# Kernel optimization log

Measured on AMD Instinct MI355X. Metric: run time of the kernel, lower is better.

Reference implementation:

```python
import jax, jax.numpy as jnp
import numpy as np

B, S, D = 1, 2048, 1024
E, F, TOP_K = 8, 2048, 2
LN_EPS = 1e-5


def setup_inputs() -> dict:
    key = jax.random.key(0)
    ks = jax.random.split(key, 8)
    sc_in = 1.0 / np.sqrt(D)
    sc_hid = 1.0 / np.sqrt(F)
    return {
        "x": jax.random.normal(ks[0], (B, S, D), dtype=jnp.float32),
        "Wr": jax.random.normal(ks[1], (D, E), dtype=jnp.float32) * sc_in,
        "br": jnp.zeros((E,), dtype=jnp.float32),
        "W1": jax.random.normal(ks[2], (E, D, F), dtype=jnp.float32) * sc_in,
        "b1": jnp.zeros((E, F), dtype=jnp.float32),
        "W2": jax.random.normal(ks[3], (E, F, D), dtype=jnp.float32) * sc_hid,
        "b2": jnp.zeros((E, D), dtype=jnp.float32),
        "gamma": jnp.ones((D,), dtype=jnp.float32),
        "beta": jnp.zeros((D,), dtype=jnp.float32),
    }


def reference(x, Wr, br, W1, b1, W2, b2, gamma, beta):
    # x: (B, S, D)
    xf = x.reshape(-1, D)  # (T, D), T = B*S
    # Router: softmax over expert logits, then top-k scores/indices.
    probs = jax.nn.softmax(xf @ Wr + br, axis=-1)           # (T, E)
    scores, idx = jax.lax.top_k(probs, TOP_K)               # (T, K)
    # combine[t, e] = sum_k scores[t, k] * [idx[t, k] == e]  (weighted scatter)
    onehot = jax.nn.one_hot(idx, E, dtype=xf.dtype)         # (T, K, E)
    combine = jnp.einsum('tk,tke->te', scores, onehot)      # (T, E)
    # Per-expert FFN, weighted scatter-add combine. Tokens not routed to an
    # expert have combine weight 0 -> identical math to masked gather/scatter.
    out = jnp.zeros_like(xf)
    for e in range(E):  # E is a small static constant
        h = jax.nn.gelu(xf @ W1[e] + b1[e])                 # (T, F)
        out = out + combine[:, e:e + 1] * (h @ W2[e] + b2[e])
    # Residual + LayerNorm (dropout = 0)
    y = x + out.reshape(B, S, D)
    mu = jnp.mean(y, axis=-1, keepdims=True)
    var = jnp.mean(jnp.square(y - mu), axis=-1, keepdims=True)
    return (y - mu) * jax.lax.rsqrt(var + LN_EPS) * gamma + beta
```

## Files before the change

### kernel.cpp

```cpp
#include <hip/hip_runtime.h>

#define T_TOK 2048
#define DDIM  1024
#define EEXP  8
#define FDIM  2048

typedef __attribute__((ext_vector_type(8))) short bf16x8;
typedef __attribute__((ext_vector_type(4))) float f32x4;
typedef __attribute__((ext_vector_type(4))) unsigned short u16x4;

__device__ __forceinline__ unsigned short f2bf(float f) {
  union { float f; unsigned int u; } v; v.f = f;
  unsigned int r = v.u + 0x7FFF + ((v.u >> 16) & 1);
  return (unsigned short)(r >> 16);
}
__device__ __forceinline__ float gelu_tanh(float x) {
  const float c = 0.7978845608028654f;
  float t = c * (x + 0.044715f * x * x * x);
  return 0.5f * x * (1.0f + tanhf(t));
}
__device__ __forceinline__ void gload_lds16(const void* g, void* lds) {
  __builtin_amdgcn_global_load_lds(
      (const __attribute__((address_space(1))) void*)g,
      (__attribute__((address_space(3))) void*)lds, 16, 0, 0);
}

__global__ __launch_bounds__(256)
void router_kernel(const float* __restrict__ x, const float* __restrict__ Wr,
                   const float* __restrict__ br, float* __restrict__ combine,
                   unsigned short* __restrict__ xbf) {
  int t = blockIdx.x;
  int tid = threadIdx.x;
  float acc[EEXP];
#pragma unroll
  for (int e = 0; e < EEXP; ++e) acc[e] = 0.f;
  const float* xr = x + (size_t)t * DDIM;
  unsigned short* xbr = xbf + (size_t)t * DDIM;
  for (int d = tid; d < DDIM; d += 256) {
    float xv = xr[d];
    xbr[d] = f2bf(xv);
    const float* w = Wr + d * EEXP;
#pragma unroll
    for (int e = 0; e < EEXP; ++e) acc[e] += xv * w[e];
  }
#pragma unroll
  for (int e = 0; e < EEXP; ++e)
    for (int off = 32; off > 0; off >>= 1) acc[e] += __shfl_down(acc[e], off);
  __shared__ float red[4][EEXP];
  int wave = tid >> 6, lane = tid & 63;
  if (lane == 0)
#pragma unroll
    for (int e = 0; e < EEXP; ++e) red[wave][e] = acc[e];
  __syncthreads();
  if (tid == 0) {
    float l[EEXP];
#pragma unroll
    for (int e = 0; e < EEXP; ++e)
      l[e] = red[0][e] + red[1][e] + red[2][e] + red[3][e] + br[e];
    int i0 = 0;
    for (int e = 1; e < EEXP; ++e) if (l[e] > l[i0]) i0 = e;
    int i1 = -1;
    for (int e = 0; e < EEXP; ++e) {
      if (e == i0) continue;
      if (i1 < 0 || l[e] > l[i1]) i1 = e;
    }
    float m = l[0];
    for (int e = 1; e < EEXP; ++e) m = fmaxf(m, l[e]);
    float p[EEXP], s = 0.f;
#pragma unroll
    for (int e = 0; e < EEXP; ++e) { p[e] = __expf(l[e] - m); s += p[e]; }
    float inv = 1.0f / s;
#pragma unroll
    for (int e = 0; e < EEXP; ++e)
      combine[t * EEXP + e] = (e == i0 || e == i1) ? p[e] * inv : 0.0f;
  }
}

__global__ __launch_bounds__(512)
void compact_kernel(const float* __restrict__ combine, int* __restrict__ idx,
                    int* __restrict__ meta) {
  int e = threadIdx.x >> 6, lane = threadIdx.x & 63;
  int cnt = 0;
  for (int t0 = 0; t0 < T_TOK; t0 += 64) {
    int t = t0 + lane;
    bool f = combine[t * EEXP + e] != 0.0f;
    unsigned long long m = __ballot(f);
    if (f) idx[e * T_TOK + cnt + __popcll(m & ((1ull << lane) - 1))] = t;
    cnt += __popcll(m);
  }
  __shared__ int sc[EEXP];
  if (lane == 0) sc[e] = cnt;
  __syncthreads();
  if (threadIdx.x == 0) {
    int b = 0;
    for (int i = 0; i < EEXP; ++i) { meta[i] = sc[i]; meta[8 + i] = b; b += sc[i]; }
    meta[16] = b;
  }
}

__global__ __launch_bounds__(256)
void wconv_kernel(const float* __restrict__ W1, const float* __restrict__ W2,
                  unsigned short* __restrict__ W1t, unsigned short* __restrict__ W2t) {
  __shared__ float tile[32][33];
  int z = blockIdx.z;
  const float* in; unsigned short* out; int R, C;
  if (z < 8) { in = W1 + (size_t)z * DDIM * FDIM; out = W1t + (size_t)z * DDIM * FDIM; R = DDIM; C = FDIM; }
  else       { in = W2 + (size_t)(z - 8) * DDIM * FDIM; out = W2t + (size_t)(z - 8) * DDIM * FDIM; R = FDIM; C = DDIM; }
  int tilesC = C >> 5;
  int tr = blockIdx.x / tilesC, tc = blockIdx.x % tilesC;
  int r0 = tr << 5, c0 = tc << 5;
  int t = threadIdx.x;
  int lr = t >> 3, lc4 = (t & 7) << 2;
  const float4 v = *(const float4*)(in + (size_t)(r0 + lr) * C + c0 + lc4);
  tile[lr][lc4 + 0] = v.x; tile[lr][lc4 + 1] = v.y;
  tile[lr][lc4 + 2] = v.z; tile[lr][lc4 + 3] = v.w;
  __syncthreads();
  u16x4 o;
  o[0] = f2bf(tile[lc4 + 0][lr]);
  o[1] = f2bf(tile[lc4 + 1][lr]);
  o[2] = f2bf(tile[lc4 + 2][lr]);
  o[3] = f2bf(tile[lc4 + 3][lr]);
  *(u16x4*)(out + (size_t)(c0 + lr) * R + r0 + lc4) = o;
}

template<int EPI>
__global__ __launch_bounds__(256)
void gemm_kernel(const unsigned short* __restrict__ A,
                 const unsigned short* __restrict__ Ball,
                 const float* __restrict__ ball,
                 const float* __restrict__ combine,
                 const int* __restrict__ idx,
                 const int* __restrict__ meta,
                 unsigned short* __restrict__ Hc,
                 float* __restrict__ accum) {
  constexpr int KF = (EPI == 0) ? DDIM : FDIM;
  constexpr int N  = (EPI == 0) ? FDIM : DDIM;
  constexpr int NT = 16;
  __shared__ unsigned short Asub[2 * 128 * 64];
  __shared__ unsigned short Bsub[2 * 128 * 64];

  int id = blockIdx.x;
  int a = id >> 7, rem = id & 127;
  int mtile = rem >> 3, b = rem & 7;
  int ne = a * 8 + b;
  int nsl = ne & 15, e = ne >> 4;
  int ntile, kbeg;
  if (EPI == 0) { ntile = nsl; kbeg = 0; }
  else          { ntile = nsl & 7; kbeg = (nsl >> 3) * 1024; }

  int cnt = meta[e];
  int m0 = mtile << 7;
  if (m0 >= cnt) return;
  int base = meta[8 + e];
  const unsigned short* B = Ball + (size_t)e * KF * N;
  const float* bias = ball + (size_t)e * N;
  int n0 = ntile << 7;
  int tid = threadIdx.x, wave = tid >> 6, lane = tid & 63;
  int wm = wave >> 1, wn = wave & 1;
  int lr = lane & 15, lk = lane >> 4;

  int arow[4], brow[4], scol[4];
#pragma unroll
  for (int i = 0; i < 4; ++i) {
    int phys = i * 4096 + wave * 1024 + lane * 16;
    int row = phys >> 7;
    int lc = (phys & 127) ^ ((row & 7) << 4);
    scol[i] = lc >> 1;
    int lrow = min(m0 + row, cnt - 1);
    arow[i] = (EPI == 0) ? idx[e * T_TOK + lrow] : (base + lrow);
    brow[i] = n0 + row;
  }

  auto stage = [&](int buf, int kt) {
#pragma unroll
    for (int i = 0; i < 4; ++i) {
      gload_lds16(A + (size_t)arow[i] * KF + kt + scol[i],
                  (char*)Asub + buf * 16384 + i * 4096 + wave * 1024);
      gload_lds16(B + (size_t)brow[i] * KF + kt + scol[i],
                  (char*)Bsub + buf * 16384 + i * 4096 + wave * 1024);
    }
  };

  f32x4 acc[4][4] = {};
  stage(0, kbeg);
  __syncthreads();
  int cur = 0;
  for (int t = 0; t < NT; ++t) {
    if (t + 1 < NT) stage(cur ^ 1, kbeg + (t + 1) * 64);
#pragma unroll
    for (int ks = 0; ks < 2; ++ks) {
      bf16x8 af[4], bf_[4];
#pragma unroll
      for (int m = 0; m < 4; ++m) {
        int row = wm * 64 + m * 16 + lr;
        int cb = (ks * 64 + lk * 16) ^ ((row & 7) << 4);
        af[m] = *(const bf16x8*)((const char*)Asub + cur * 16384 + row * 128 + cb);
      }
#pragma unroll
      for (int n = 0; n < 4; ++n) {
        int row = wn * 64 + n * 16 + lr;
        int cb = (ks * 64 + lk * 16) ^ ((row & 7) << 4);
        bf_[n] = *(const bf16x8*)((const char*)Bsub + cur * 16384 + row * 128 + cb);
      }
#pragma unroll
      for (int m = 0; m < 4; ++m)
#pragma unroll
        for (int n = 0; n < 4; ++n)
          acc[m][n] = __builtin_amdgcn_mfma_f32_16x16x32_bf16(af[m], bf_[n], acc[m][n], 0, 0, 0);
    }
    __syncthreads();
    cur ^= 1;
  }

  if (EPI == 0) {
#pragma unroll
    for (int m = 0; m < 4; ++m) {
      int lbase = m0 + wm * 64 + m * 16 + lk * 4;
#pragma unroll
      for (int n = 0; n < 4; ++n) {
        int col = n0 + wn * 64 + n * 16 + lr;
        float bv = bias[col];
#pragma unroll
        for (int r = 0; r < 4; ++r) {
          int local = lbase + r;
          if (local < cnt)
            Hc[(size_t)(base + local) * N + col] = f2bf(gelu_tanh(acc[m][n][r] + bv));
        }
      }
    }
  } else {
    bool addb = (kbeg == 0);
#pragma unroll
    for (int m = 0; m < 4; ++m) {
      int lbase = m0 + wm * 64 + m * 16 + lk * 4;
#pragma unroll
      for (int r = 0; r < 4; ++r) {
        int local = lbase + r;
        if (local < cnt) {
          int tok = idx[e * T_TOK + local];
          float c = combine[tok * EEXP + e];
#pragma unroll
          for (int n = 0; n < 4; ++n) {
            int col = n0 + wn * 64 + n * 16 + lr;
            float v = acc[m][n][r] + (addb ? bias[col] : 0.0f);
            atomicAdd(&accum[(size_t)tok * N + col], c * v);
          }
        }
      }
    }
  }
}

__global__ __launch_bounds__(256)
void ln_kernel(const float* __restrict__ x, const float* __restrict__ accum,
               const float* __restrict__ gamma, const float* __restrict__ beta,
               float* __restrict__ out) {
  int r = blockIdx.x, tid = threadIdx.x;
  size_t base = (size_t)r * DDIM + tid * 4;
  float4 xv = *(const float4*)(x + base);
  float4 av = *(const float4*)(accum + base);
  float y[4] = { xv.x + av.x, xv.y + av.y, xv.z + av.z, xv.w + av.w };
  float s = y[0] + y[1] + y[2] + y[3];
  float s2 = y[0] * y[0] + y[1] * y[1] + y[2] * y[2] + y[3] * y[3];
  for (int off = 32; off > 0; off >>= 1) {
    s += __shfl_down(s, off);
    s2 += __shfl_down(s2, off);
  }
  __shared__ float rs[4], rs2[4];
  int wave = tid >> 6, lane = tid & 63;
  if (lane == 0) { rs[wave] = s; rs2[wave] = s2; }
  __syncthreads();
  float ts = rs[0] + rs[1] + rs[2] + rs[3];
  float ts2 = rs2[0] + rs2[1] + rs2[2] + rs2[3];
  float mu = ts * (1.0f / DDIM);
  float var = ts2 * (1.0f / DDIM) - mu * mu;
  float inv = rsqrtf(var + 1e-5f);
  float4 gv = *(const float4*)(gamma + tid * 4);
  float4 bv = *(const float4*)(beta + tid * 4);
  float4 o;
  o.x = (y[0] - mu) * inv * gv.x + bv.x;
  o.y = (y[1] - mu) * inv * gv.y + bv.y;
  o.z = (y[2] - mu) * inv * gv.z + bv.z;
  o.w = (y[3] - mu) * inv * gv.w + bv.w;
  *(float4*)(out + base) = o;
}

#define BM 128
#define BN 128
#define BK 32
#define LDT 40

__global__ __launch_bounds__(256)
void g1_old(const float* __restrict__ X, const float* __restrict__ W1,
            const float* __restrict__ b1, unsigned short* __restrict__ H) {
  __shared__ unsigned short As[BM][LDT];
  __shared__ unsigned short Bs[BN][LDT];
  int tid = threadIdx.x;
  int trow0 = blockIdx.y * BM, ncol0 = blockIdx.x * BN;
  int wave = tid >> 6, lane = tid & 63;
  int wm = wave >> 1, wn = wave & 1;
  int lr = lane & 15, lk = lane >> 4;
  f32x4 acc[4][4] = {};
  for (int kt = 0; kt < DDIM; kt += BK) {
#pragma unroll
    for (int it = 0; it < 4; ++it) {
      int i = tid + it * 256;
      int row = i >> 3, c4 = (i & 7) << 2;
      const float4 v = *(const float4*)(X + (size_t)(trow0 + row) * DDIM + kt + c4);
      uint2 p;
      p.x = (unsigned int)f2bf(v.x) | ((unsigned int)f2bf(v.y) << 16);
      p.y = (unsigned int)f2bf(v.z) | ((unsigned int)f2bf(v.w) << 16);
      *(uint2*)&As[row][c4] = p;
    }
#pragma unroll
    for (int it = 0; it < 4; ++it) {
      int i = tid + it * 256;
      int r = i >> 5, c4 = (i & 31) << 2;
      const float4 v = *(const float4*)(W1 + (size_t)(kt + r) * FDIM + ncol0 + c4);
      Bs[c4 + 0][r] = f2bf(v.x); Bs[c4 + 1][r] = f2bf(v.y);
      Bs[c4 + 2][r] = f2bf(v.z); Bs[c4 + 3][r] = f2bf(v.w);
    }
    __syncthreads();
    bf16x8 af[4], bfr[4];
#pragma unroll
    for (int m = 0; m < 4; ++m) af[m] = *(const bf16x8*)&As[wm * 64 + m * 16 + lr][lk * 8];
#pragma unroll
    for (int n = 0; n < 4; ++n) bfr[n] = *(const bf16x8*)&Bs[wn * 64 + n * 16 + lr][lk * 8];
#pragma unroll
    for (int m = 0; m < 4; ++m)
#pragma unroll
      for (int n = 0; n < 4; ++n)
        acc[m][n] = __builtin_amdgcn_mfma_f32_16x16x32_bf16(af[m], bfr[n], acc[m][n], 0, 0, 0);
    __syncthreads();
  }
#pragma unroll
  for (int m = 0; m < 4; ++m) {
    int row = trow0 + wm * 64 + m * 16 + lk * 4;
#pragma unroll
    for (int n = 0; n < 4; ++n) {
      int col = ncol0 + wn * 64 + n * 16 + lr;
      float bv = b1[col];
#pragma unroll
      for (int r = 0; r < 4; ++r)
        H[(size_t)(row + r) * FDIM + col] = f2bf(gelu_tanh(acc[m][n][r] + bv));
    }
  }
}

__global__ __launch_bounds__(256)
void g2_old(const unsigned short* __restrict__ H, const float* __restrict__ W2,
            const float* __restrict__ b2, const float* __restrict__ combine,
            int e, float* __restrict__ out) {
  __shared__ unsigned short As[BM][LDT];
  __shared__ unsigned short Bs[BN][LDT];
  int tid = threadIdx.x;
  int trow0 = blockIdx.y * BM, ncol0 = blockIdx.x * BN;
  int wave = tid >> 6, lane = tid & 63;
  int wm = wave >> 1, wn = wave & 1;
  int lr = lane & 15, lk = lane >> 4;
  f32x4 acc[4][4] = {};
  for (int kt = 0; kt < FDIM; kt += BK) {
#pragma unroll
    for (int it = 0; it < 2; ++it) {
      int i = tid + it * 256;
      int row = i >> 2, c8 = (i & 3) << 3;
      uint4 v = *(const uint4*)(H + (size_t)(trow0 + row) * FDIM + kt + c8);
      *(uint4*)&As[row][c8] = v;
    }
#pragma unroll
    for (int it = 0; it < 4; ++it) {
      int i = tid + it * 256;
      int r = i >> 5, c4 = (i & 31) << 2;
      const float4 v = *(const float4*)(W2 + (size_t)(kt + r) * DDIM + ncol0 + c4);
      Bs[c4 + 0][r] = f2bf(v.x); Bs[c4 + 1][r] = f2bf(v.y);
      Bs[c4 + 2][r] = f2bf(v.z); Bs[c4 + 3][r] = f2bf(v.w);
    }
    __syncthreads();
    bf16x8 af[4], bfr[4];
#pragma unroll
    for (int m = 0; m < 4; ++m) af[m] = *(const bf16x8*)&As[wm * 64 + m * 16 + lr][lk * 8];
#pragma unroll
    for (int n = 0; n < 4; ++n) bfr[n] = *(const bf16x8*)&Bs[wn * 64 + n * 16 + lr][lk * 8];
#pragma unroll
    for (int m = 0; m < 4; ++m)
#pragma unroll
      for (int n = 0; n < 4; ++n)
        acc[m][n] = __builtin_amdgcn_mfma_f32_16x16x32_bf16(af[m], bfr[n], acc[m][n], 0, 0, 0);
    __syncthreads();
  }
#pragma unroll
  for (int m = 0; m < 4; ++m) {
    int row = trow0 + wm * 64 + m * 16 + lk * 4;
#pragma unroll
    for (int n = 0; n < 4; ++n) {
      int col = ncol0 + wn * 64 + n * 16 + lr;
      float bv = b2[col];
#pragma unroll
      for (int r = 0; r < 4; ++r) {
        int rr = row + r;
        float c = combine[rr * EEXP + e];
        if (c != 0.0f) out[(size_t)rr * DDIM + col] += c * (acc[m][n][r] + bv);
      }
    }
  }
}

extern "C" void kernel_launch(void* const* d_in, const int* in_sizes, int n_in,
                              void* d_out, int out_size, void* d_ws, size_t ws_size,
                              hipStream_t stream) {
  const float* x     = (const float*)d_in[0];
  const float* Wr    = (const float*)d_in[1];
  const float* br    = (const float*)d_in[2];
  const float* W1    = (const float*)d_in[3];
  const float* b1    = (const float*)d_in[4];
  const float* W2    = (const float*)d_in[5];
  const float* b2    = (const float*)d_in[6];
  const float* gamma = (const float*)d_in[7];
  const float* beta  = (const float*)d_in[8];

  size_t off_combine = 0;
  size_t off_meta    = off_combine + (size_t)T_TOK * EEXP * 4;
  size_t off_idx     = off_meta + 1024;
  size_t off_xbf     = off_idx + (size_t)EEXP * T_TOK * 4;
  size_t off_accum   = off_xbf + (size_t)T_TOK * DDIM * 2;
  size_t off_Hc      = off_accum + (size_t)T_TOK * DDIM * 4;
  size_t off_W1t     = off_Hc + (size_t)2 * T_TOK * FDIM * 2;
  size_t off_W2t     = off_W1t + (size_t)EEXP * DDIM * FDIM * 2;
  size_t need        = off_W2t + (size_t)EEXP * DDIM * FDIM * 2;

  float* combine = (float*)((char*)d_ws + off_combine);

  if (ws_size >= need) {
    int*   meta  = (int*)((char*)d_ws + off_meta);
    int*   idx   = (int*)((char*)d_ws + off_idx);
    unsigned short* xbf = (unsigned short*)((char*)d_ws + off_xbf);
    float* accum = (float*)((char*)d_ws + off_accum);
    unsigned short* Hc  = (unsigned short*)((char*)d_ws + off_Hc);
    unsigned short* W1t = (unsigned short*)((char*)d_ws + off_W1t);
    unsigned short* W2t = (unsigned short*)((char*)d_ws + off_W2t);

    wconv_kernel<<<dim3(2048, 1, 16), 256, 0, stream>>>(W1, W2, W1t, W2t);
    router_kernel<<<T_TOK, 256, 0, stream>>>(x, Wr, br, combine, xbf);
    compact_kernel<<<1, 512, 0, stream>>>(combine, idx, meta);
    hipMemsetAsync(accum, 0, (size_t)T_TOK * DDIM * 4, stream);
    gemm_kernel<0><<<2048, 256, 0, stream>>>(xbf, W1t, b1, combine, idx, meta, Hc, nullptr);
    gemm_kernel<1><<<2048, 256, 0, stream>>>(Hc, W2t, b2, combine, idx, meta, nullptr, accum);
    ln_kernel<<<T_TOK, 256, 0, stream>>>(x, accum, gamma, beta, (float*)d_out);
  } else {
    float* accum = (float*)((char*)d_ws + off_xbf);
    unsigned short* Hbf = (unsigned short*)(accum + (size_t)T_TOK * DDIM);
    hipMemsetAsync(accum, 0, (size_t)T_TOK * DDIM * 4, stream);
    router_kernel<<<T_TOK, 256, 0, stream>>>(x, Wr, br, combine, Hbf );
    for (int e = 0; e < EEXP; ++e) {
      g1_old<<<dim3(FDIM / BN, T_TOK / BM), 256, 0, stream>>>(
          x, W1 + (size_t)e * DDIM * FDIM, b1 + (size_t)e * FDIM, Hbf);
      g2_old<<<dim3(DDIM / BN, T_TOK / BM), 256, 0, stream>>>(
          Hbf, W2 + (size_t)e * FDIM * DDIM, b2 + (size_t)e * DDIM, combine, e, accum);
    }
    ln_kernel<<<T_TOK, 256, 0, stream>>>(x, accum, gamma, beta, (float*)d_out);
  }
}
```

Baseline: 355.6 us.

## Use compacted 64-row expert tiles and single-buffer LDS in MoE GEMMs

The compact kernel now emits prefix sums of 64-row tile counts per expert, so the GEMM grid covers only occupied tiles instead of launching a fixed 2048 blocks with early exits. The M tile shrinks from 128 to 64 rows, which cuts padding waste on partially filled expert tiles. The LDS double buffer is removed, so each k-step loads and then syncs with no prefetch overlap. This lowers LDS use and may raise occupancy, but it gives up load/compute overlap and halves A-tile reuse per block.

```diff
diff --git a/kernel.cpp b/kernel.cpp
--- a/kernel.cpp
+++ b/kernel.cpp
@@ -92,9 +92,12 @@
   if (lane == 0) sc[e] = cnt;
   __syncthreads();
   if (threadIdx.x == 0) {
-    int b = 0;
-    for (int i = 0; i < EEXP; ++i) { meta[i] = sc[i]; meta[8 + i] = b; b += sc[i]; }
-    meta[16] = b;
+    int b = 0, tb = 0;
+    for (int i = 0; i < EEXP; ++i) {
+      meta[i] = sc[i]; meta[8 + i] = b; meta[24 + i] = tb;
+      b += sc[i]; tb += (sc[i] + 63) >> 6;
+    }
+    meta[16] = b; meta[17] = tb;
   }
 }
 
@@ -136,86 +139,87 @@
   constexpr int KF = (EPI == 0) ? DDIM : FDIM;
   constexpr int N  = (EPI == 0) ? FDIM : DDIM;
   constexpr int NT = 16;
-  __shared__ unsigned short Asub[2 * 128 * 64];
-  __shared__ unsigned short Bsub[2 * 128 * 64];
+  __shared__ unsigned short Asub[64 * 64];
+  __shared__ unsigned short Bsub[128 * 64];
 
   int id = blockIdx.x;
-  int a = id >> 7, rem = id & 127;
-  int mtile = rem >> 3, b = rem & 7;
-  int ne = a * 8 + b;
-  int nsl = ne & 15, e = ne >> 4;
-  int ntile, kbeg;
-  if (EPI == 0) { ntile = nsl; kbeg = 0; }
-  else          { ntile = nsl & 7; kbeg = (nsl >> 3) * 1024; }
-
+  int tile = id >> 4, sub = id & 15;
+  if (tile >= meta[17]) return;
+  int e = 0;
+#pragma unroll
+  for (int i = 1; i < 8; ++i) if (tile >= meta[24 + i]) e = i;
+  int m0 = (tile - meta[24 + e]) << 6;
   int cnt = meta[e];
-  int m0 = mtile << 7;
-  if (m0 >= cnt) return;
   int base = meta[8 + e];
+  int n0, kbeg;
+  if (EPI == 0) { n0 = sub << 7; kbeg = 0; }
+  else          { n0 = (sub >> 1) << 7; kbeg = (sub & 1) << 10; }
+
   const unsigned short* B = Ball + (size_t)e * KF * N;
   const float* bias = ball + (size_t)e * N;
-  int n0 = ntile << 7;
   int tid = threadIdx.x, wave = tid >> 6, lane = tid & 63;
   int wm = wave >> 1, wn = wave & 1;
   int lr = lane & 15, lk = lane >> 4;
 
-  int arow[4], brow[4], scol[4];
+  int arow[2], scolA[2], brow[4], scolB[4];
+#pragma unroll
+  for (int i = 0; i < 2; ++i) {
+    int phys = i * 4096 + wave * 1024 + lane * 16;
+    int row = phys >> 7;
+    int lc = (phys & 127) ^ ((row & 7) << 4);
+    scolA[i] = lc >> 1;
+    int lrow = min(m0 + row, cnt - 1);
+    arow[i] = (EPI == 0) ? idx[e * T_TOK + lrow] : (base + lrow);
+  }
 #pragma unroll
   for (int i = 0; i < 4; ++i) {
     int phys = i * 4096 + wave * 1024 + lane * 16;
     int row = phys >> 7;
     int lc = (phys & 127) ^ ((row & 7) << 4);
-    scol[i] = lc >> 1;
-    int lrow = min(m0 + row, cnt - 1);
-    arow[i] = (EPI == 0) ? idx[e * T_TOK + lrow] : (base + lrow);
+    scolB[i] = lc >> 1;
     brow[i] = n0 + row;
   }
 
-  auto stage = [&](int buf, int kt) {
-#pragma unroll
-    for (int i = 0; i < 4; ++i) {
-      gload_lds16(A + (size_t)arow[i] * KF + kt + scol[i],
-                  (char*)Asub + buf * 16384 + i * 4096 + wave * 1024);
-      gload_lds16(B + (size_t)brow[i] * KF + kt + scol[i],
-                  (char*)Bsub + buf * 16384 + i * 4096 + wave * 1024);
-    }
-  };
-
-  f32x4 acc[4][4] = {};
-  stage(0, kbeg);
-  __syncthreads();
-  int cur = 0;
+  f32x4 acc[2][4] = {};
   for (int t = 0; t < NT; ++t) {
-    if (t + 1 < NT) stage(cur ^ 1, kbeg + (t + 1) * 64);
+    int kt = kbeg + t * 64;
+#pragma unroll
+    for (int i = 0; i < 2; ++i)
+      gload_lds16(A + (size_t)arow[i] * KF + kt + scolA[i],
+                  (char*)Asub + i * 4096 + wave * 1024);
+#pragma unroll
+    for (int i = 0; i < 4; ++i)
+      gload_lds16(B + (size_t)brow[i] * KF + kt + scolB[i],
+                  (char*)Bsub + i * 4096 + wave * 1024);
+    __syncthreads();
 #pragma unroll
     for (int ks = 0; ks < 2; ++ks) {
-      bf16x8 af[4], bf_[4];
-#pragma unroll
-      for (int m = 0; m < 4; ++m) {
-        int row = wm * 64 + m * 16 + lr;
+      bf16x8 af[2], bf_[4];
+#pragma unroll
+      for (int m = 0; m < 2; ++m) {
+        int row = wm * 32 + m * 16 + lr;
         int cb = (ks * 64 + lk * 16) ^ ((row & 7) << 4);
-        af[m] = *(const bf16x8*)((const char*)Asub + cur * 16384 + row * 128 + cb);
+        af[m] = *(const bf16x8*)((const char*)Asub + row * 128 + cb);
       }
 #pragma unroll
       for (int n = 0; n < 4; ++n) {
         int row = wn * 64 + n * 16 + lr;
         int cb = (ks * 64 + lk * 16) ^ ((row & 7) << 4);
-        bf_[n] = *(const bf16x8*)((const char*)Bsub + cur * 16384 + row * 128 + cb);
+        bf_[n] = *(const bf16x8*)((const char*)Bsub + row * 128 + cb);
       }
 #pragma unroll
-      for (int m = 0; m < 4; ++m)
+      for (int m = 0; m < 2; ++m)
 #pragma unroll
         for (int n = 0; n < 4; ++n)
           acc[m][n] = __builtin_amdgcn_mfma_f32_16x16x32_bf16(af[m], bf_[n], acc[m][n], 0, 0, 0);
     }
     __syncthreads();
-    cur ^= 1;
   }
 
   if (EPI == 0) {
 #pragma unroll
-    for (int m = 0; m < 4; ++m) {
-      int lbase = m0 + wm * 64 + m * 16 + lk * 4;
+    for (int m = 0; m < 2; ++m) {
+      int lbase = m0 + wm * 32 + m * 16 + lk * 4;
 #pragma unroll
       for (int n = 0; n < 4; ++n) {
         int col = n0 + wn * 64 + n * 16 + lr;
@@ -231,8 +235,8 @@
   } else {
     bool addb = (kbeg == 0);
 #pragma unroll
-    for (int m = 0; m < 4; ++m) {
-      int lbase = m0 + wm * 64 + m * 16 + lk * 4;
+    for (int m = 0; m < 2; ++m) {
+      int lbase = m0 + wm * 32 + m * 16 + lk * 4;
 #pragma unroll
       for (int r = 0; r < 4; ++r) {
         int local = lbase + r;
@@ -443,8 +447,8 @@
     router_kernel<<<T_TOK, 256, 0, stream>>>(x, Wr, br, combine, xbf);
     compact_kernel<<<1, 512, 0, stream>>>(combine, idx, meta);
     hipMemsetAsync(accum, 0, (size_t)T_TOK * DDIM * 4, stream);
-    gemm_kernel<0><<<2048, 256, 0, stream>>>(xbf, W1t, b1, combine, idx, meta, Hc, nullptr);
-    gemm_kernel<1><<<2048, 256, 0, stream>>>(Hc, W2t, b2, combine, idx, meta, nullptr, accum);
+    gemm_kernel<0><<<72 * 16, 256, 0, stream>>>(xbf, W1t, b1, combine, idx, meta, Hc, nullptr);
+    gemm_kernel<1><<<72 * 16, 256, 0, stream>>>(Hc, W2t, b2, combine, idx, meta, nullptr, accum);
     ln_kernel<<<T_TOK, 256, 0, stream>>>(x, accum, gamma, beta, (float*)d_out);
   } else {
     float* accum = (float*)((char*)d_ws + off_xbf);
```

New measurement: 309.9 us. -12.9%, faster.
